# Kernel optimization log

Measured on AMD Instinct MI355X. Metric: run time of the kernel, lower is better.

The kernel has to match this reference:

```python
import jax, jax.numpy as jnp
import numpy as np

SEQ = 4096
E = 2048

def setup_inputs() -> dict:
    key = jax.random.key(0)
    kx, kq, kk, kv = jax.random.split(key, 4)
    scale = 1.0 / np.sqrt(E)
    x = jax.random.normal(kx, (SEQ, E), dtype=jnp.float32)
    # nn.Linear weights: shape [out, in], applied as x @ W.T
    Wq = jax.random.uniform(kq, (E, E), dtype=jnp.float32, minval=-scale, maxval=scale)
    Wk = jax.random.uniform(kk, (E, E), dtype=jnp.float32, minval=-scale, maxval=scale)
    Wv = jax.random.uniform(kv, (E, E), dtype=jnp.float32, minval=-scale, maxval=scale)
    return {"x": x, "Wq": Wq, "Wk": Wk, "Wv": Wv}

def reference(x, Wq, Wk, Wv):
    # q/k/v projections: nn.Linear(bias=False) -> x @ W.T
    q = x @ Wq.T  # [S, E]
    k = x @ Wk.T  # [S, E]
    v = x @ Wv.T  # [S, E]
    s = q @ k.T  # [S, S]
    w = jax.nn.softmax(s / jnp.sqrt(jnp.float32(E)), axis=-1)
    return w @ v  # [S, E]
```

## Files before the change

### kernel.cpp

```cpp
#include <hip/hip_runtime.h>
#include <hip/hip_bf16.h>

#define S_DIM 4096
#define E_DIM 2048

typedef __attribute__((ext_vector_type(4))) float f32x4;
typedef __attribute__((ext_vector_type(8))) short bf16x8;

__device__ __forceinline__ unsigned short f2bf(float f) {
  unsigned u = __builtin_bit_cast(unsigned, f);
  u += 0x7FFFu + ((u >> 16) & 1u);
  return (unsigned short)(u >> 16);
}
__device__ __forceinline__ float bf2f(unsigned short h) {
  return __builtin_bit_cast(float, ((unsigned)h) << 16);
}

__global__ __launch_bounds__(256) void cast_kernel(const float* __restrict__ in,
                                                   unsigned short* __restrict__ out,
                                                   int n4) {
  int i = blockIdx.x * 256 + threadIdx.x;
  if (i >= n4) return;
  float4 v = reinterpret_cast<const float4*>(in)[i];
  ushort4 o;
  o.x = f2bf(v.x); o.y = f2bf(v.y); o.z = f2bf(v.z); o.w = f2bf(v.w);
  reinterpret_cast<ushort4*>(out)[i] = o;
}

__global__ __launch_bounds__(256) void add_kernel(const float* __restrict__ a,
                                                  const float* __restrict__ b,
                                                  float* __restrict__ o, int n4) {
  int i = blockIdx.x * 256 + threadIdx.x;
  if (i >= n4) return;
  float4 va = reinterpret_cast<const float4*>(a)[i];
  float4 vb = reinterpret_cast<const float4*>(b)[i];
  float4 vo = {va.x + vb.x, va.y + vb.y, va.z + vb.z, va.w + vb.w};
  reinterpret_cast<float4*>(o)[i] = vo;
}


__device__ __forceinline__ void stage_half(const unsigned short* __restrict__ g,
                                           int grow0, int ld, int kByte0,
                                           char* ldsHalfBase, int tid) {
#pragma unroll
  for (int p = 0; p < 2; ++p) {
    const int o = (p * 512 + tid) * 16;
    const int S = o >> 10;
    const int oi = o & 1023;
    const int osi = oi ^ (((oi >> 9) & 1) << 5);
    const int r  = (S >> 1) * 16 + (osi >> 6);
    const int cb = (S & 1) * 64 + (osi & 63);
    const char* ga = reinterpret_cast<const char*>(g) +
                     ((size_t)(grow0 + r) * ld) * 2 + kByte0 + cb;
    char* la = ldsHalfBase + (o & ~1023);
    __builtin_amdgcn_global_load_lds(
        (const __attribute__((address_space(1))) void*)ga,
        (__attribute__((address_space(3))) void*)la, 16, 0, 0);
  }
}

#define MFMA_QUAD(AM, AN, AF, BF)                                              \
  _Pragma("unroll") for (int mm = 0; mm < 4; ++mm)                             \
  _Pragma("unroll") for (int nn = 0; nn < 2; ++nn)                             \
  _Pragma("unroll") for (int ks = 0; ks < 2; ++ks)                             \
    acc[(AM) + mm][(AN) + nn] = __builtin_amdgcn_mfma_f32_16x16x32_bf16(       \
        AF[mm][ks], BF[nn][ks], acc[(AM) + mm][(AN) + nn], 0, 0, 0);

enum { EPI_QKV = 0, EPI_BF16 = 1, EPI_F32 = 2 };

template <int EPI>
__global__ __launch_bounds__(512, 2) void gemm8(
    const unsigned short* __restrict__ A, const unsigned short* __restrict__ B,
    int lda, int ldb, int K,
    float* __restrict__ Cf, unsigned short* __restrict__ Cb,
    unsigned short* __restrict__ Ct, int ldc, float scale,
    int kElemPerZ, long long zStrideC) {
  extern __shared__ char lds[];

  const int tid = threadIdx.x;
  const int rowA0 = blockIdx.y * 256;
  const int rowB0 = blockIdx.x * 256;
  const int k0B = blockIdx.z * kElemPerZ * 2;
  if (EPI == EPI_F32) Cf += (size_t)blockIdx.z * zStrideC;

  const int wave = tid >> 6;
  const int lane = tid & 63;
  const int wm = wave >> 2;
  const int wn = wave & 3;
  const int l15 = lane & 15;
  const int kg = lane >> 4;
  const int rsw = (l15 * 64 + kg * 16) ^ ((l15 & 8) << 2);

  int bSub[2][2];
#pragma unroll
  for (int nh = 0; nh < 2; ++nh)
#pragma unroll
    for (int nn = 0; nn < 2; ++nn) {
      const int row = wn * 64 + nh * 32 + nn * 16;
      bSub[nh][nn] = 32768 + (row >> 7) * 16384 + ((row & 127) >> 4) * 2048;
    }
  const int aBase = wm * 16384;

  f32x4 acc[8][4];
#pragma unroll
  for (int mi = 0; mi < 8; ++mi)
#pragma unroll
    for (int ni = 0; ni < 4; ++ni) acc[mi][ni] = (f32x4){0.f, 0.f, 0.f, 0.f};

  const int NT = K / 64;
  char* buf0 = lds;
  char* buf1 = lds + 65536;

  stage_half(A, rowA0,       lda, k0B,       buf0 + 0,     tid);
  stage_half(A, rowA0 + 128, lda, k0B,       buf0 + 16384, tid);
  stage_half(B, rowB0,       ldb, k0B,       buf0 + 32768, tid);
  stage_half(B, rowB0 + 128, ldb, k0B,       buf0 + 49152, tid);
  stage_half(A, rowA0,       lda, k0B + 128, buf1 + 0,     tid);
  stage_half(A, rowA0 + 128, lda, k0B + 128, buf1 + 16384, tid);
  stage_half(B, rowB0,       ldb, k0B + 128, buf1 + 32768, tid);
  asm volatile("s_waitcnt vmcnt(6)" ::: "memory");
  __builtin_amdgcn_sched_barrier(0);
  __builtin_amdgcn_s_barrier();

  for (int t = 0; t < NT; ++t) {
    char* bufc = lds + (t & 1) * 65536;
    char* bufn = lds + ((t & 1) ^ 1) * 65536;
    bf16x8 a0[4][2], a1[4][2], b0[2][2], b1[2][2];

#pragma unroll
    for (int mm = 0; mm < 4; ++mm)
#pragma unroll
      for (int ks = 0; ks < 2; ++ks)
        a0[mm][ks] = *reinterpret_cast<const bf16x8*>(
            bufc + aBase + (mm * 2 + ks) * 1024 + rsw);
#pragma unroll
    for (int nn = 0; nn < 2; ++nn)
#pragma unroll
      for (int ks = 0; ks < 2; ++ks)
        b0[nn][ks] = *reinterpret_cast<const bf16x8*>(
            bufc + bSub[0][nn] + ks * 1024 + rsw);
    if (t + 1 < NT)
      stage_half(B, rowB0 + 128, ldb, k0B + (t + 1) * 128, bufn + 49152, tid);
    asm volatile("s_waitcnt lgkmcnt(8)" ::: "memory");
    __builtin_amdgcn_s_barrier();
    asm volatile("s_waitcnt lgkmcnt(0)" ::: "memory");
    __builtin_amdgcn_sched_barrier(0);
    __builtin_amdgcn_s_setprio(1);
    MFMA_QUAD(0, 0, a0, b0)
    __builtin_amdgcn_s_setprio(0);
    __builtin_amdgcn_s_barrier();

#pragma unroll
    for (int nn = 0; nn < 2; ++nn)
#pragma unroll
      for (int ks = 0; ks < 2; ++ks)
        b1[nn][ks] = *reinterpret_cast<const bf16x8*>(
            bufc + bSub[1][nn] + ks * 1024 + rsw);
    __builtin_amdgcn_s_barrier();
    asm volatile("s_waitcnt lgkmcnt(0)" ::: "memory");
    __builtin_amdgcn_sched_barrier(0);
    __builtin_amdgcn_s_setprio(1);
    MFMA_QUAD(0, 2, a0, b1)
    __builtin_amdgcn_s_setprio(0);
    __builtin_amdgcn_s_barrier();

#pragma unroll
    for (int mm = 0; mm < 4; ++mm)
#pragma unroll
      for (int ks = 0; ks < 2; ++ks)
        a1[mm][ks] = *reinterpret_cast<const bf16x8*>(
            bufc + aBase + ((4 + mm) * 2 + ks) * 1024 + rsw);
    __builtin_amdgcn_s_barrier();
    asm volatile("s_waitcnt lgkmcnt(0)" ::: "memory");
    __builtin_amdgcn_sched_barrier(0);
    __builtin_amdgcn_s_setprio(1);
    MFMA_QUAD(4, 2, a1, b1)
    __builtin_amdgcn_s_setprio(0);
    __builtin_amdgcn_s_barrier();

    if (t + 2 < NT) {
      const int kb = k0B + (t + 2) * 128;
      stage_half(A, rowA0,       lda, kb, bufc + 0,     tid);
      stage_half(A, rowA0 + 128, lda, kb, bufc + 16384, tid);
      stage_half(B, rowB0,       ldb, kb, bufc + 32768, tid);
      asm volatile("s_waitcnt vmcnt(6)" ::: "memory");
    } else {
      asm volatile("s_waitcnt vmcnt(0)" ::: "memory");
    }
    __builtin_amdgcn_sched_barrier(0);
    __builtin_amdgcn_s_barrier();
    __builtin_amdgcn_s_setprio(1);
    MFMA_QUAD(4, 0, a1, b0)
    __builtin_amdgcn_s_setprio(0);
    __builtin_amdgcn_s_barrier();
  }

  const int r0 = rowA0 + wm * 128;
  const int c0 = rowB0 + wn * 64;
#pragma unroll
  for (int mi = 0; mi < 8; ++mi) {
    const int row = r0 + (mi >> 2) * 64 + (mi & 3) * 16 + kg * 4;
#pragma unroll
    for (int ni = 0; ni < 4; ++ni) {
      const int col = c0 + (ni >> 1) * 32 + (ni & 1) * 16 + l15;
      f32x4 v = acc[mi][ni];
      if constexpr (EPI == EPI_F32) {
#pragma unroll
        for (int r = 0; r < 4; ++r)
          Cf[(size_t)(row + r) * ldc + col] = v[r];
      } else if constexpr (EPI == EPI_BF16) {
#pragma unroll
        for (int r = 0; r < 4; ++r)
          Cb[(size_t)(row + r) * ldc + col] = f2bf(v[r] * scale);
      } else {
        if (rowB0 < 4096) {
#pragma unroll
          for (int r = 0; r < 4; ++r)
            Cb[(size_t)(row + r) * 4096 + col] = f2bf(v[r]);
        } else {
          ushort4 pk;
          pk.x = f2bf(v[0]); pk.y = f2bf(v[1]);
          pk.z = f2bf(v[2]); pk.w = f2bf(v[3]);
          *reinterpret_cast<ushort4*>(Ct + (size_t)(col - 4096) * 4096 + row) = pk;
        }
      }
    }
  }
}

__global__ __launch_bounds__(256) void softmax_kernel(const unsigned short* __restrict__ Sm,
                                                      unsigned short* __restrict__ P) {
  const int row = blockIdx.x;
  const int tid = threadIdx.x;
  const unsigned short* src = Sm + (size_t)row * S_DIM;
  float vals[16];
  float mx = -1e30f;
#pragma unroll
  for (int i = 0; i < 4; ++i) {
    ushort4 h = reinterpret_cast<const ushort4*>(src)[tid + i * 256];
    float a = bf2f(h.x), b = bf2f(h.y), c = bf2f(h.z), d = bf2f(h.w);
    vals[i * 4 + 0] = a; vals[i * 4 + 1] = b;
    vals[i * 4 + 2] = c; vals[i * 4 + 3] = d;
    mx = fmaxf(mx, fmaxf(fmaxf(a, b), fmaxf(c, d)));
  }
#pragma unroll
  for (int off = 32; off >= 1; off >>= 1) mx = fmaxf(mx, __shfl_xor(mx, off, 64));
  __shared__ float red[8];
  const int wave = tid >> 6, lane = tid & 63;
  if (lane == 0) red[wave] = mx;
  __syncthreads();
  mx = fmaxf(fmaxf(red[0], red[1]), fmaxf(red[2], red[3]));
  float sum = 0.f;
#pragma unroll
  for (int i = 0; i < 16; ++i) { vals[i] = __expf(vals[i] - mx); sum += vals[i]; }
#pragma unroll
  for (int off = 32; off >= 1; off >>= 1) sum += __shfl_xor(sum, off, 64);
  if (lane == 0) red[4 + wave] = sum;
  __syncthreads();
  sum = red[4] + red[5] + red[6] + red[7];
  const float inv = 1.0f / sum;
  unsigned short* dst = P + (size_t)row * S_DIM;
#pragma unroll
  for (int i = 0; i < 4; ++i) {
    ushort4 pk;
    pk.x = f2bf(vals[i * 4 + 0] * inv);
    pk.y = f2bf(vals[i * 4 + 1] * inv);
    pk.z = f2bf(vals[i * 4 + 2] * inv);
    pk.w = f2bf(vals[i * 4 + 3] * inv);
    reinterpret_cast<ushort4*>(dst)[tid + i * 256] = pk;
  }
}

extern "C" void kernel_launch(void* const* d_in, const int* in_sizes, int n_in,
                              void* d_out, int out_size, void* d_ws, size_t ws_size,
                              hipStream_t stream) {
  const float* x  = (const float*)d_in[0];
  const float* Wq = (const float*)d_in[1];
  const float* Wk = (const float*)d_in[2];
  const float* Wv = (const float*)d_in[3];
  float* out = (float*)d_out;
  char* ws = (char*)d_ws;

  const size_t MB = 1024 * 1024;
  const size_t NEED = 120 * MB;
  if (ws_size < NEED) return;

  unsigned short* xb   = (unsigned short*)(ws);
  unsigned short* wcat = (unsigned short*)(ws + 16 * MB);
  unsigned short* qkb  = (unsigned short*)(ws + 40 * MB);
  unsigned short* vt   = (unsigned short*)(ws + 72 * MB);
  unsigned short* Sb   = (unsigned short*)(ws + 88 * MB);
  float* outp0 = (float*)(ws);
  float* outp1 = (float*)(ws + 88 * MB);
  unsigned short* P = qkb;

  hipFuncSetAttribute(reinterpret_cast<const void*>(&gemm8<EPI_QKV>),
                      hipFuncAttributeMaxDynamicSharedMemorySize, 131072);
  hipFuncSetAttribute(reinterpret_cast<const void*>(&gemm8<EPI_BF16>),
                      hipFuncAttributeMaxDynamicSharedMemorySize, 131072);
  hipFuncSetAttribute(reinterpret_cast<const void*>(&gemm8<EPI_F32>),
                      hipFuncAttributeMaxDynamicSharedMemorySize, 131072);

  const int nx4 = S_DIM * E_DIM / 4;
  const int nw4 = E_DIM * E_DIM / 4;

  cast_kernel<<<nx4 / 256, 256, 0, stream>>>(x, xb, nx4);
  cast_kernel<<<nw4 / 256, 256, 0, stream>>>(Wq, wcat, nw4);
  cast_kernel<<<nw4 / 256, 256, 0, stream>>>(Wk, wcat + (size_t)2048 * 2048, nw4);
  cast_kernel<<<nw4 / 256, 256, 0, stream>>>(Wv, wcat + (size_t)4096 * 2048, nw4);

  gemm8<EPI_QKV><<<dim3(24, 16, 1), 512, 131072, stream>>>(
      xb, wcat, E_DIM, E_DIM, E_DIM, nullptr, qkb, vt, 4096, 1.0f, 0, 0);

  const float scale = 0.022097086912079608f;
  gemm8<EPI_BF16><<<dim3(16, 16, 1), 512, 131072, stream>>>(
      qkb, qkb + 2048, 4096, 4096, E_DIM, nullptr, Sb, nullptr, 4096, scale, 0, 0);

  softmax_kernel<<<S_DIM, 256, 0, stream>>>(Sb, P);

  gemm8<EPI_F32><<<dim3(8, 16, 2), 512, 131072, stream>>>(
      P, vt, 4096, 4096, 2048, outp0, nullptr, nullptr, E_DIM, 1.0f,
      2048, (long long)(88 * MB) / 4);

  add_kernel<<<nx4 / 256, 256, 0, stream>>>(outp0, outp1, out, nx4);
}
```

Measured before the change: 418.4 us.

## Restructure GEMM prefetch schedule, add XCD-aware block remap, fuse weight casts

Three unrelated changes. The GEMM kernel now remaps workgroup IDs so that consecutive tiles land on the same XCD chiplet, aiming for better L2 reuse. It also reorders the global-to-LDS staging so both B halves for tile t+2 are issued earlier, right after the a1 fragment loads, with the waitcnt thresholds adjusted to match. The three weight cast launches are merged into a single kernel to cut launch overhead. The remap assumes the grid size divides evenly by 8, and the new prefetch timing could conflict with LDS reads still in flight from the current buffer.

New measurement: 404.4 us. 1.03x faster.

```diff
diff --git a/kernel.cpp b/kernel.cpp
--- a/kernel.cpp
+++ b/kernel.cpp
@@ -22,6 +22,21 @@
   int i = blockIdx.x * 256 + threadIdx.x;
   if (i >= n4) return;
   float4 v = reinterpret_cast<const float4*>(in)[i];
+  ushort4 o;
+  o.x = f2bf(v.x); o.y = f2bf(v.y); o.z = f2bf(v.z); o.w = f2bf(v.w);
+  reinterpret_cast<ushort4*>(out)[i] = o;
+}
+
+__global__ __launch_bounds__(256) void cast3_kernel(const float* __restrict__ w0,
+                                                    const float* __restrict__ w1,
+                                                    const float* __restrict__ w2,
+                                                    unsigned short* __restrict__ out,
+                                                    int n4each) {
+  int i = blockIdx.x * 256 + threadIdx.x;
+  if (i >= 3 * n4each) return;
+  const float* src = (i < n4each) ? w0 : (i < 2 * n4each ? w1 : w2);
+  int j = (i < n4each) ? i : (i < 2 * n4each ? i - n4each : i - 2 * n4each);
+  float4 v = reinterpret_cast<const float4*>(src)[j];
   ushort4 o;
   o.x = f2bf(v.x); o.y = f2bf(v.y); o.z = f2bf(v.z); o.w = f2bf(v.w);
   reinterpret_cast<ushort4*>(out)[i] = o;
@@ -78,8 +93,17 @@
   extern __shared__ char lds[];
 
   const int tid = threadIdx.x;
-  const int rowA0 = blockIdx.y * 256;
-  const int rowB0 = blockIdx.x * 256;
+  int bx = blockIdx.x, by = blockIdx.y;
+  {
+    const int gx = gridDim.x;
+    const int nwg = gx * gridDim.y;
+    const int orig = by * gx + bx;
+    const int q = nwg >> 3;
+    const int s = (orig & 7) * q + (orig >> 3);
+    bx = s % gx; by = s / gx;
+  }
+  const int rowA0 = by * 256;
+  const int rowB0 = bx * 256;
   const int k0B = blockIdx.z * kElemPerZ * 2;
   if (EPI == EPI_F32) Cf += (size_t)blockIdx.z * zStrideC;
 
@@ -115,16 +139,16 @@
   stage_half(A, rowA0 + 128, lda, k0B,       buf0 + 16384, tid);
   stage_half(B, rowB0,       ldb, k0B,       buf0 + 32768, tid);
   stage_half(B, rowB0 + 128, ldb, k0B,       buf0 + 49152, tid);
+  stage_half(B, rowB0,       ldb, k0B + 128, buf1 + 32768, tid);
+  stage_half(B, rowB0 + 128, ldb, k0B + 128, buf1 + 49152, tid);
   stage_half(A, rowA0,       lda, k0B + 128, buf1 + 0,     tid);
   stage_half(A, rowA0 + 128, lda, k0B + 128, buf1 + 16384, tid);
-  stage_half(B, rowB0,       ldb, k0B + 128, buf1 + 32768, tid);
-  asm volatile("s_waitcnt vmcnt(6)" ::: "memory");
+  asm volatile("s_waitcnt vmcnt(8)" ::: "memory");
   __builtin_amdgcn_sched_barrier(0);
   __builtin_amdgcn_s_barrier();
 
   for (int t = 0; t < NT; ++t) {
     char* bufc = lds + (t & 1) * 65536;
-    char* bufn = lds + ((t & 1) ^ 1) * 65536;
     bf16x8 a0[4][2], a1[4][2], b0[2][2], b1[2][2];
 
 #pragma unroll
@@ -139,8 +163,6 @@
       for (int ks = 0; ks < 2; ++ks)
         b0[nn][ks] = *reinterpret_cast<const bf16x8*>(
             bufc + bSub[0][nn] + ks * 1024 + rsw);
-    if (t + 1 < NT)
-      stage_half(B, rowB0 + 128, ldb, k0B + (t + 1) * 128, bufn + 49152, tid);
     asm volatile("s_waitcnt lgkmcnt(8)" ::: "memory");
     __builtin_amdgcn_s_barrier();
     asm volatile("s_waitcnt lgkmcnt(0)" ::: "memory");
@@ -170,6 +192,11 @@
       for (int ks = 0; ks < 2; ++ks)
         a1[mm][ks] = *reinterpret_cast<const bf16x8*>(
             bufc + aBase + ((4 + mm) * 2 + ks) * 1024 + rsw);
+    if (t + 2 < NT) {
+      const int kb = k0B + (t + 2) * 128;
+      stage_half(B, rowB0,       ldb, kb, bufc + 32768, tid);
+      stage_half(B, rowB0 + 128, ldb, kb, bufc + 49152, tid);
+    }
     __builtin_amdgcn_s_barrier();
     asm volatile("s_waitcnt lgkmcnt(0)" ::: "memory");
     __builtin_amdgcn_sched_barrier(0);
@@ -182,8 +209,7 @@
       const int kb = k0B + (t + 2) * 128;
       stage_half(A, rowA0,       lda, kb, bufc + 0,     tid);
       stage_half(A, rowA0 + 128, lda, kb, bufc + 16384, tid);
-      stage_half(B, rowB0,       ldb, kb, bufc + 32768, tid);
-      asm volatile("s_waitcnt vmcnt(6)" ::: "memory");
+      asm volatile("s_waitcnt vmcnt(8)" ::: "memory");
     } else {
       asm volatile("s_waitcnt vmcnt(0)" ::: "memory");
     }
@@ -305,9 +331,7 @@
   const int nw4 = E_DIM * E_DIM / 4;
 
   cast_kernel<<<nx4 / 256, 256, 0, stream>>>(x, xb, nx4);
-  cast_kernel<<<nw4 / 256, 256, 0, stream>>>(Wq, wcat, nw4);
-  cast_kernel<<<nw4 / 256, 256, 0, stream>>>(Wk, wcat + (size_t)2048 * 2048, nw4);
-  cast_kernel<<<nw4 / 256, 256, 0, stream>>>(Wv, wcat + (size_t)4096 * 2048, nw4);
+  cast3_kernel<<<3 * nw4 / 256, 256, 0, stream>>>(Wq, Wk, Wv, wcat, nw4);
 
   gemm8<EPI_QKV><<<dim3(24, 16, 1), 512, 131072, stream>>>(
       xb, wcat, E_DIM, E_DIM, E_DIM, nullptr, qkb, vt, 4096, 1.0f, 0, 0);
```
